# Kernel optimization log

Hardware: AMD Instinct MI355X
Metric: run time of the kernel (lower is better)

Reference implementation:

```python
import jax, jax.numpy as jnp
import numpy as np

B, NA, LAT, HID, AF, L = 512, 58, 64, 128, 10, 2
N = B * NA
E = N * 16


def silu(x):
    return x * jax.nn.sigmoid(x)


def setup_inputs() -> dict:
    key = jax.random.key(0)
    ks = list(jax.random.split(key, 32))

    def p(k, shape, fan_in):
        return jax.random.normal(k, shape, jnp.float32) / np.sqrt(fan_in)

    inp = {
        "z": jax.random.normal(ks[0], (B, LAT), jnp.float32),
        "atom_types": jax.random.uniform(ks[1], (N, AF), jnp.float32),
        "edge_index": jax.random.randint(ks[2], (2, E), 0, N, jnp.int64),
        "init_coords": jax.random.normal(ks[3], (NA, 3), jnp.float32) * 0.1,
        "latent_w": p(ks[4], (LAT, HID), LAT), "latent_b": jnp.zeros((HID,), jnp.float32),
        "atom_w": p(ks[5], (AF, HID), AF), "atom_b": jnp.zeros((HID,), jnp.float32),
        # per-layer stacked params (leading dim = num_layers)
        "edge_w1": p(ks[6], (L, 2 * HID + 1, HID), 2 * HID + 1), "edge_b1": jnp.zeros((L, HID), jnp.float32),
        "edge_w2": p(ks[7], (L, HID, HID), HID), "edge_b2": jnp.zeros((L, HID), jnp.float32),
        "node_w1": p(ks[8], (L, 2 * HID, HID), 2 * HID), "node_b1": jnp.zeros((L, HID), jnp.float32),
        "node_w2": p(ks[9], (L, HID, HID), HID), "node_b2": jnp.zeros((L, HID), jnp.float32),
        "coord_w1": p(ks[10], (L, HID, HID), HID), "coord_b1": jnp.zeros((L, HID), jnp.float32),
        "coord_w2": p(ks[11], (L, HID, 1), HID),  # no bias
        "ln_g": jnp.ones((L, HID), jnp.float32), "ln_b": jnp.zeros((L, HID), jnp.float32),
        "head_w1": p(ks[12], (HID, HID // 2), HID), "head_b1": jnp.zeros((HID // 2,), jnp.float32),
        "head_w2": p(ks[13], (HID // 2, 3), HID // 2), "head_b2": jnp.zeros((3,), jnp.float32),
    }
    return inp


def _layer(h, pos, row, col, ew1, eb1, ew2, eb2, nw1, nb1, nw2, nb2, cw1, cb1, cw2, lg, lb):
    n = h.shape[0]
    xi, xj = h[row], h[col]                      # [E,HID] gathers
    rel = pos[row] - pos[col]                    # [E,3]
    d2 = jnp.clip(jnp.sum(rel * rel, axis=-1, keepdims=True), 1e-6, 1e6)
    ef = jnp.concatenate([xi, xj, d2], axis=-1)  # [E,2H+1]
    m = silu(silu(ef @ ew1 + eb1) @ ew2 + eb2)   # edge MLP messages [E,HID]
    agg = jax.ops.segment_sum(m, row, num_segments=n)
    hn = silu(jnp.concatenate([h, agg], axis=-1) @ nw1 + nb1) @ nw2 + nb2
    mu = jnp.mean(hn, axis=-1, keepdims=True)
    var = jnp.mean((hn - mu) ** 2, axis=-1, keepdims=True)
    hn = (hn - mu) * jax.lax.rsqrt(var + 1e-5) * lg + lb
    cw = jnp.clip(silu(m @ cw1 + cb1) @ cw2, -1.0, 1.0)  # [E,1]
    upd = jax.ops.segment_sum(cw * rel, row, num_segments=n)  # [N,3]
    deg = jax.ops.segment_sum(jnp.ones((row.shape[0],), pos.dtype), row, num_segments=n)[:, None]
    pos_new = pos + upd / (deg + 1e-6)
    return hn, pos_new


def reference(z, atom_types, edge_index, init_coords, latent_w, latent_b, atom_w, atom_b,
              edge_w1, edge_b1, edge_w2, edge_b2, node_w1, node_b1, node_w2, node_b2,
              coord_w1, coord_b1, coord_w2, ln_g, ln_b, head_w1, head_b1, head_w2, head_b2):
    b = z.shape[0]
    na = init_coords.shape[0]
    n = b * na
    h = z @ latent_w + latent_b                              # [B,HID]
    h = jnp.broadcast_to(h[:, None, :], (b, na, h.shape[-1])).reshape(n, -1)
    h = h + (atom_types @ atom_w + atom_b)
    pos = jnp.broadcast_to(init_coords[None], (b, na, 3)).reshape(n, 3)
    row, col = edge_index[0], edge_index[1]
    for l in range(edge_w1.shape[0]):
        h, pos = _layer(h, pos, row, col,
                        edge_w1[l], edge_b1[l], edge_w2[l], edge_b2[l],
                        node_w1[l], node_b1[l], node_w2[l], node_b2[l],
                        coord_w1[l], coord_b1[l], coord_w2[l], ln_g[l], ln_b[l])
    delta = silu(h @ head_w1 + head_b1) @ head_w2 + head_b2
    return pos + delta
```

## Files before the change

kernel.cpp:

```cpp
#include <hip/hip_runtime.h>
#include <hip/hip_bf16.h>

#define BB 512
#define NA 58
#define LAT 64
#define HID 128
#define AF 10
#define NL 2
#define NN (BB*NA)
#define NE (NN*16)
#define ET 64
#define NTILE (NE/ET)
#define PBLK 768

typedef __attribute__((ext_vector_type(8))) short s8;
typedef __attribute__((ext_vector_type(4))) float f4;

struct CvtDesc {
    const void* src[24];
    float*      dst[24];
    int         len[24];
};

struct PackJobs {
    const float* src[10];
    short*       dst[10];
    int          K[10];
    int          mode[10];
};

__device__ __forceinline__ float siluf(float x) {
    return x * __builtin_amdgcn_rcpf(1.0f + __expf(-x));
}

__device__ __forceinline__ short f2b(float x) {
    __hip_bfloat16 b = __float2bfloat16(x);
    return *(short*)&b;
}

__device__ __forceinline__ float b2f(short s) {
    return __uint_as_float(((unsigned int)(unsigned short)s) << 16);
}

__global__ void k_detect(const unsigned short* __restrict__ z16,
                         const unsigned int* __restrict__ e32,
                         int* __restrict__ flags) {
    __shared__ int sbf, si64;
    if (threadIdx.x == 0) { sbf = 0; si64 = 0; }
    __syncthreads();
    int c1 = 0, c2 = 0;
    for (int i = threadIdx.x; i < 1024; i += 256) {
        unsigned short v = z16[2*i];
        int e = (v >> 7) & 0xFF;
        if (e >= 100 && e <= 140) c1++;
        if (e32[2*i + 1] == 0u) c2++;
    }
    atomicAdd(&sbf, c1);
    atomicAdd(&si64, c2);
    __syncthreads();
    if (threadIdx.x == 0) {
        flags[0] = (sbf  > 600) ? 1 : 0;
        flags[1] = (si64 > 600) ? 1 : 0;
    }
}

__global__ void k_convert(CvtDesc d, const int* __restrict__ flags) {
    int a = blockIdx.y;
    int i = blockIdx.x * blockDim.x + threadIdx.x;
    int n = d.len[a];
    if (i >= n) return;
    if (flags[0]) {
        d.dst[a][i] = __bfloat162float(((const __hip_bfloat16*)d.src[a])[i]);
    } else {
        d.dst[a][i] = ((const float*)d.src[a])[i];
    }
}

__global__ void k_packall(PackJobs pj) {
    int j = blockIdx.y;
    int idx = blockIdx.x * 256 + threadIdx.x;
    const float* w = pj.src[j];
    short* o = pj.dst[j];
    if (pj.mode[j] == 0) {
        int K = pj.K[j];
        if (idx >= 128*K) return;
        int jj = idx & 7;
        int l  = (idx >> 3) & 63;
        int rest = idx >> 9;
        int KC = K >> 5;
        int kc = rest % KC;
        int nt = rest / KC;
        int n = nt*16 + (l & 15);
        int k = kc*32 + (l >> 4)*8 + jj;
        o[idx] = f2b(w[k*128 + n]);
    } else {
        if (idx >= 32768) return;
        int jj = idx & 7;
        int l  = (idx >> 3) & 63;
        int rest = idx >> 9;
        int kc = rest & 3;
        int nt = rest >> 2;
        int n = nt*16 + (l & 15);
        int k = kc*32 + (l >> 4)*8 + jj;
        float v = (n < 128) ? w[k*128 + n] : w[(128 + k)*128 + (n - 128)];
        o[idx] = f2b(v);
    }
}

__global__ void k_hist(const int* __restrict__ eidx, const int* __restrict__ flags,
                       int* __restrict__ cnt) {
    int e = blockIdx.x * 256 + threadIdx.x;
    if (e >= NE) return;
    int is64 = flags[1];
    int r = eidx[is64 ? 2*(long)e : (long)e];
    atomicAdd(&cnt[r], 1);
}

__global__ __launch_bounds__(1024) void k_scan(const int* __restrict__ cnt,
                                               int* __restrict__ rowStart,
                                               int* __restrict__ cursor) {
    __shared__ int part[1024];
    int t = threadIdx.x;
    int base = t * 29;
    int loc[29];
    int s = 0;
    #pragma unroll
    for (int i = 0; i < 29; ++i) { loc[i] = s; s += cnt[base + i]; }
    part[t] = s;
    __syncthreads();
    for (int d = 1; d < 1024; d <<= 1) {
        int v = (t >= d) ? part[t - d] : 0;
        __syncthreads();
        part[t] += v;
        __syncthreads();
    }
    int pre = (t == 0) ? 0 : part[t - 1];
    #pragma unroll
    for (int i = 0; i < 29; ++i) {
        int v = pre + loc[i];
        rowStart[base + i] = v;
        cursor[base + i] = v;
    }
    if (t == 1023) rowStart[NN] = pre + s;
}

__global__ void k_scatter(const int* __restrict__ eidx, const int* __restrict__ flags,
                          int* __restrict__ cursor,
                          int* __restrict__ rS, int* __restrict__ cS) {
    int e = blockIdx.x * 256 + threadIdx.x;
    if (e >= NE) return;
    int is64 = flags[1];
    long ge = e, gc = (long)e + NE;
    int r = eidx[is64 ? 2*ge : ge];
    int c = eidx[is64 ? 2*gc : gc];
    int p = atomicAdd(&cursor[r], 1);
    rS[p] = r; cS[p] = c;
}

__global__ void k_hz(const float* __restrict__ z, const float* __restrict__ lw,
                     const float* __restrict__ lb, float* __restrict__ hz) {
    __shared__ float zs[LAT];
    int b = blockIdx.x;
    int c = threadIdx.x;
    if (c < LAT) zs[c] = z[b*LAT + c];
    __syncthreads();
    float acc = lb[c];
    #pragma unroll
    for (int k = 0; k < LAT; ++k) acc += zs[k] * lw[k*HID + c];
    hz[b*HID + c] = acc;
}

__global__ void k_init2(const float* __restrict__ hz, const float* __restrict__ at,
                        const float* __restrict__ aw, const float* __restrict__ ab,
                        const float* __restrict__ ic,
                        float* __restrict__ pos, short* __restrict__ hb) {
    __shared__ float ats[AF];
    int n = blockIdx.x;
    int c = threadIdx.x;
    int b = n / NA;
    if (c < AF) ats[c] = at[n*AF + c];
    __syncthreads();
    float acc = hz[b*HID + c] + ab[c];
    #pragma unroll
    for (int f = 0; f < AF; ++f) acc += ats[f] * aw[f*HID + c];
    hb[(long)n*HID + c] = f2b(acc);
    if (c < 3) {
        int a = n % NA;
        pos[n*3 + c] = ic[a*3 + c];
    }
}

__global__ __launch_bounds__(256) void k_pre(
    const short* __restrict__ hb, const short* __restrict__ wcat,
    const float* __restrict__ b1, short* __restrict__ H1,
    float* __restrict__ agg, float* __restrict__ upd)
{
    __shared__ short x[64][136];
    const int tid = threadIdx.x;
    const int n0 = blockIdx.x * 64;

    {
        long base = (long)blockIdx.x*256 + tid;
        f4* a4 = (f4*)agg;
        for (long j = base; j < (long)NN*HID/4; j += (long)gridDim.x*256) a4[j] = (f4)0.f;
        if (base < NN*3) upd[base] = 0.f;
    }

    #pragma unroll
    for (int it = 0; it < 4; ++it) {
        int idx = it*256 + tid;
        int e = idx >> 4, q = idx & 15;
        *(int4*)&x[e][q*8] = *(const int4*)(hb + (long)(n0+e)*HID + q*8);
    }
    __syncthreads();

    const int l = tid & 63, w = tid >> 6;
    const int l16 = l & 15, quad = l >> 4;

    f4 acc[4][4];
    #pragma unroll
    for (int mt = 0; mt < 4; ++mt)
        #pragma unroll
        for (int nt4 = 0; nt4 < 4; ++nt4) acc[mt][nt4] = (f4)0.f;

    #pragma unroll
    for (int kc = 0; kc < 4; ++kc) {
        s8 a[4];
        #pragma unroll
        for (int mt = 0; mt < 4; ++mt)
            a[mt] = *(const s8*)&x[mt*16 + l16][kc*32 + quad*8];
        #pragma unroll
        for (int nt4 = 0; nt4 < 4; ++nt4) {
            int nt = w*4 + nt4;
            s8 b = *(const s8*)(wcat + (((size_t)nt*4 + kc)*64 + l)*8);
            #pragma unroll
            for (int mt = 0; mt < 4; ++mt)
                acc[mt][nt4] = __builtin_amdgcn_mfma_f32_16x16x32_bf16(a[mt], b, acc[mt][nt4], 0, 0, 0);
        }
    }
    #pragma unroll
    for (int nt4 = 0; nt4 < 4; ++nt4) {
        int col = (w*4 + nt4)*16 + l16;
        float bias = (col < 128) ? b1[col] : 0.f;
        #pragma unroll
        for (int mt = 0; mt < 4; ++mt)
            #pragma unroll
            for (int i = 0; i < 4; ++i) {
                int row = mt*16 + quad*4 + i;
                H1[(long)(n0 + row)*256 + col] = f2b(acc[mt][nt4][i] + bias);
            }
    }
}

__global__ __launch_bounds__(256, 3) void k_edge7(
    const short* __restrict__ H1,
    const int* __restrict__ rS, const int* __restrict__ cS,
    const float* __restrict__ pos,
    const float* __restrict__ w1c,
    const short* __restrict__ w2p, const float* __restrict__ b2,
    const short* __restrict__ c1p, const float* __restrict__ cb1,
    const float* __restrict__ cw2,
    float* __restrict__ agg, float* __restrict__ upd)
{
    __shared__ short t1[ET][136];
    __shared__ short mm[ET][136];
    __shared__ int   rIs[ET], cIs[ET];
    __shared__ float sred[ET];

    const int tid = threadIdx.x;
    const int l = tid & 63, w = tid >> 6;
    const int l16 = l & 15, quad = l >> 4;
    const int c0 = (2*w)*16 + l16, c1c = (2*w+1)*16 + l16;
    const int half = tid >> 7, ch = tid & 127;
    const int q = tid & 15;
    const int esub = tid >> 4;

    float wv[8];
    #pragma unroll
    for (int j = 0; j < 8; ++j) wv[j] = w1c[q*8 + j];

    s8 w2f[8], c1f[8];
    #pragma unroll
    for (int kc = 0; kc < 4; ++kc) {
        w2f[kc]     = *(const s8*)(w2p + (((size_t)(2*w)*4 + kc)*64 + l)*8);
        w2f[4 + kc] = *(const s8*)(w2p + (((size_t)(2*w+1)*4 + kc)*64 + l)*8);
        c1f[kc]     = *(const s8*)(c1p + (((size_t)(2*w)*4 + kc)*64 + l)*8);
        c1f[4 + kc] = *(const s8*)(c1p + (((size_t)(2*w+1)*4 + kc)*64 + l)*8);
    }
    const float bia2_0 = b2[c0],  bia2_1 = b2[c1c];
    const float biac_0 = cb1[c0], biac_1 = cb1[c1c];
    const float cw0    = cw2[c0], cw1v   = cw2[c1c];

    int   pri[4], pci[4];
    float pd2[4];

    auto PREIDX = [&](int T) {
        long eb = (long)T * ET;
        #pragma unroll
        for (int it = 0; it < 4; ++it) {
            int e = esub + 16*it;
            int r = rS[eb + e], c = cS[eb + e];
            pri[it] = r; pci[it] = c;
            float rx = pos[r*3+0] - pos[c*3+0];
            float ry = pos[r*3+1] - pos[c*3+1];
            float rz = pos[r*3+2] - pos[c*3+2];
            pd2[it] = fminf(fmaxf(rx*rx + ry*ry + rz*rz, 1e-6f), 1e6f);
        }
    };

    int t = blockIdx.x;
    if (t < NTILE) PREIDX(t);

    while (t < NTILE) {
        __syncthreads();
        if (tid < ET) sred[tid] = 0.f;
        if (q == 0) {
            #pragma unroll
            for (int it = 0; it < 4; ++it) {
                rIs[esub + 16*it] = pri[it];
                cIs[esub + 16*it] = pci[it];
            }
        }
        #pragma unroll
        for (int it = 0; it < 4; ++it) {
            s8 va = *(const s8*)(H1 + (long)pri[it]*256 + q*8);
            s8 vb = *(const s8*)(H1 + (long)pci[it]*256 + 128 + q*8);
            float d2 = pd2[it];
            s8 o;
            #pragma unroll
            for (int j = 0; j < 8; ++j) {
                float v = b2f(va[j]) + b2f(vb[j]) + d2*wv[j];
                o[j] = f2b(siluf(v));
            }
            *(s8*)&t1[esub + 16*it][q*8] = o;
        }
        __syncthreads();

        int tn = t + PBLK;
        if (tn < NTILE) PREIDX(tn);

        {
            f4 acc[4][2];
            #pragma unroll
            for (int mt = 0; mt < 4; ++mt) { acc[mt][0] = (f4)0.f; acc[mt][1] = (f4)0.f; }
            #pragma unroll
            for (int kc = 0; kc < 4; ++kc) {
                #pragma unroll
                for (int mt = 0; mt < 4; ++mt) {
                    s8 a = *(const s8*)&t1[mt*16 + l16][kc*32 + quad*8];
                    acc[mt][0] = __builtin_amdgcn_mfma_f32_16x16x32_bf16(a, w2f[kc],     acc[mt][0], 0, 0, 0);
                    acc[mt][1] = __builtin_amdgcn_mfma_f32_16x16x32_bf16(a, w2f[4 + kc], acc[mt][1], 0, 0, 0);
                }
            }
            #pragma unroll
            for (int mt = 0; mt < 4; ++mt) {
                #pragma unroll
                for (int i = 0; i < 4; ++i) {
                    int row = mt*16 + quad*4 + i;
                    mm[row][c0]  = f2b(siluf(acc[mt][0][i] + bia2_0));
                    mm[row][c1c] = f2b(siluf(acc[mt][1][i] + bia2_1));
                }
            }
        }
        __syncthreads();

        {
            f4 acc[4][2];
            #pragma unroll
            for (int mt = 0; mt < 4; ++mt) { acc[mt][0] = (f4)0.f; acc[mt][1] = (f4)0.f; }
            #pragma unroll
            for (int kc = 0; kc < 4; ++kc) {
                #pragma unroll
                for (int mt = 0; mt < 4; ++mt) {
                    s8 a = *(const s8*)&mm[mt*16 + l16][kc*32 + quad*8];
                    acc[mt][0] = __builtin_amdgcn_mfma_f32_16x16x32_bf16(a, c1f[kc],     acc[mt][0], 0, 0, 0);
                    acc[mt][1] = __builtin_amdgcn_mfma_f32_16x16x32_bf16(a, c1f[4 + kc], acc[mt][1], 0, 0, 0);
                }
            }
            #pragma unroll
            for (int mt = 0; mt < 4; ++mt) {
                #pragma unroll
                for (int i = 0; i < 4; ++i) {
                    float p = siluf(acc[mt][0][i] + biac_0) * cw0
                            + siluf(acc[mt][1][i] + biac_1) * cw1v;
                    p += __shfl_xor(p, 1);
                    p += __shfl_xor(p, 2);
                    p += __shfl_xor(p, 4);
                    p += __shfl_xor(p, 8);
                    if (l16 == 0) {
                        int row = mt*16 + quad*4 + i;
                        atomicAdd(&sred[row], p);
                    }
                }
            }
        }

        {
            int e0 = half * 32;
            int cur = rIs[e0];
            float a = 0.f;
            #pragma unroll
            for (int e = e0; e < e0 + 32; ++e) {
                int r = rIs[e];
                if (r != cur) {
                    atomicAdd(&agg[(long)cur*HID + ch], a);
                    a = 0.f; cur = r;
                }
                a += b2f(mm[e][ch]);
            }
            atomicAdd(&agg[(long)cur*HID + ch], a);
        }
        __syncthreads();

        if (tid < ET) {
            float cwv = fminf(fmaxf(sred[tid], -1.f), 1.f);
            int r = rIs[tid], c = cIs[tid];
            float rx = pos[r*3+0] - pos[c*3+0];
            float ry = pos[r*3+1] - pos[c*3+1];
            float rz = pos[r*3+2] - pos[c*3+2];
            atomicAdd(&upd[r*3+0], cwv*rx);
            atomicAdd(&upd[r*3+1], cwv*ry);
            atomicAdd(&upd[r*3+2], cwv*rz);
        }
        t = tn;
    }
}

__global__ __launch_bounds__(256) void k_node_mfma(
    short* __restrict__ hb, const float* __restrict__ agg,
    const short* __restrict__ w1p, const float* __restrict__ b1n,
    const short* __restrict__ w2p, const float* __restrict__ b2n,
    const float* __restrict__ lg, const float* __restrict__ lb,
    float* __restrict__ pos, const float* __restrict__ upd,
    const int* __restrict__ rowStart)
{
    __shared__ short x[64][264];
    __shared__ short t1[64][144];
    __shared__ float mus[64], rstds[64];
    float (*hn)[132] = (float (*)[132])&x[0][0];

    const int tid = threadIdx.x;
    const int n0 = blockIdx.x * 64;

    #pragma unroll
    for (int it = 0; it < 4; ++it) {
        int idx = it*256 + tid;
        int e = idx >> 4, q = idx & 15;
        *(int4*)&x[e][q*8] = *(const int4*)(hb + (long)(n0+e)*HID + q*8);
    }
    #pragma unroll
    for (int it = 0; it < 8; ++it) {
        int idx = it*256 + tid;
        int e = idx >> 5, q = idx & 31;
        float4 v = *(const float4*)(agg + (long)(n0+e)*HID + q*4);
        short4 sv;
        sv.x = f2b(v.x); sv.y = f2b(v.y); sv.z = f2b(v.z); sv.w = f2b(v.w);
        *(short4*)&x[e][128 + q*4] = sv;
    }
    __syncthreads();

    const int l = tid & 63, w = tid >> 6;
    const int l16 = l & 15, quad = l >> 4;
    const int nt0 = 2*w, nt1 = 2*w + 1;
    const int c0 = nt0*16 + l16, c1c = nt1*16 + l16;

    {
        f4 acc[4][2];
        #pragma unroll
        for (int mt = 0; mt < 4; ++mt) { acc[mt][0] = (f4)0.f; acc[mt][1] = (f4)0.f; }
        #pragma unroll
        for (int kc = 0; kc < 8; ++kc) {
            s8 b0  = *(const s8*)(w1p + (((size_t)nt0*8 + kc)*64 + l)*8);
            s8 b1f = *(const s8*)(w1p + (((size_t)nt1*8 + kc)*64 + l)*8);
            #pragma unroll
            for (int mt = 0; mt < 4; ++mt) {
                s8 a = *(const s8*)&x[mt*16 + l16][kc*32 + quad*8];
                acc[mt][0] = __builtin_amdgcn_mfma_f32_16x16x32_bf16(a, b0,  acc[mt][0], 0, 0, 0);
                acc[mt][1] = __builtin_amdgcn_mfma_f32_16x16x32_bf16(a, b1f, acc[mt][1], 0, 0, 0);
            }
        }
        float bia0 = b1n[c0], bia1 = b1n[c1c];
        #pragma unroll
        for (int mt = 0; mt < 4; ++mt) {
            #pragma unroll
            for (int i = 0; i < 4; ++i) {
                int row = mt*16 + quad*4 + i;
                t1[row][c0]  = f2b(siluf(acc[mt][0][i] + bia0));
                t1[row][c1c] = f2b(siluf(acc[mt][1][i] + bia1));
            }
        }
    }
    __syncthreads();

    {
        f4 acc[4][2];
        #pragma unroll
        for (int mt = 0; mt < 4; ++mt) { acc[mt][0] = (f4)0.f; acc[mt][1] = (f4)0.f; }
        #pragma unroll
        for (int kc = 0; kc < 4; ++kc) {
            s8 b0  = *(const s8*)(w2p + (((size_t)nt0*4 + kc)*64 + l)*8);
            s8 b1f = *(const s8*)(w2p + (((size_t)nt1*4 + kc)*64 + l)*8);
            #pragma unroll
            for (int mt = 0; mt < 4; ++mt) {
                s8 a = *(const s8*)&t1[mt*16 + l16][kc*32 + quad*8];
                acc[mt][0] = __builtin_amdgcn_mfma_f32_16x16x32_bf16(a, b0,  acc[mt][0], 0, 0, 0);
                acc[mt][1] = __builtin_amdgcn_mfma_f32_16x16x32_bf16(a, b1f, acc[mt][1], 0, 0, 0);
            }
        }
        float bia0 = b2n[c0], bia1 = b2n[c1c];
        __syncthreads();
        #pragma unroll
        for (int mt = 0; mt < 4; ++mt) {
            #pragma unroll
            for (int i = 0; i < 4; ++i) {
                int row = mt*16 + quad*4 + i;
                hn[row][c0]  = acc[mt][0][i] + bia0;
                hn[row][c1c] = acc[mt][1][i] + bia1;
            }
        }
    }
    __syncthreads();

    {
        int r = tid >> 2, part = tid & 3;
        float s = 0.f, q = 0.f;
        #pragma unroll
        for (int j = 0; j < 32; ++j) {
            float v = hn[r][part + 4*j];
            s += v; q += v*v;
        }
        s += __shfl_xor(s, 1); q += __shfl_xor(q, 1);
        s += __shfl_xor(s, 2); q += __shfl_xor(q, 2);
        if (part == 0) {
            float mu = s * (1.0f/HID);
            float var = q * (1.0f/HID) - mu*mu;
            mus[r] = mu;
            rstds[r] = rsqrtf(var + 1e-5f);
        }
    }
    __syncthreads();

    #pragma unroll
    for (int it = 0; it < 32; ++it) {
        int idx = it*256 + tid;
        int r = idx >> 7, c = idx & 127;
        float v = (hn[r][c] - mus[r]) * rstds[r] * lg[c] + lb[c];
        hb[(long)(n0 + r)*HID + c] = f2b(v);
    }
    if (tid < 192) {
        int i = tid / 3, d = tid - i*3;
        int n = n0 + i;
        float dg = (float)(rowStart[n+1] - rowStart[n]);
        pos[n*3+d] += upd[n*3+d] / (dg + 1e-6f);
    }
}

__global__ void k_head(const short* __restrict__ hb, const float* __restrict__ pos,
                       const float* __restrict__ w1, const float* __restrict__ b1,
                       const float* __restrict__ w2, const float* __restrict__ b2,
                       void* __restrict__ out, const int* __restrict__ flags)
{
    __shared__ float hs[4][HID];
    __shared__ float t[4][64];
    const int tid = threadIdx.x;
    const int n0 = blockIdx.x * 4;
    for (int i = tid; i < 4*HID; i += 256)
        hs[i >> 7][i & 127] = b2f(hb[(long)n0*HID + i]);
    __syncthreads();
    const int s = tid >> 6, c = tid & 63;
    float acc = b1[c];
    for (int k4 = 0; k4 < 32; ++k4) {
        int k = k4*4;
        float wa = w1[(k+0)*64 + c];
        float wb = w1[(k+1)*64 + c];
        float wc = w1[(k+2)*64 + c];
        float wd = w1[(k+3)*64 + c];
        float4 v = *(const float4*)&hs[s][k];
        acc += v.x*wa + v.y*wb + v.z*wc + v.w*wd;
    }
    t[s][c] = siluf(acc);
    __syncthreads();
    if (c < 3) {
        float a2 = b2[c];
        #pragma unroll
        for (int k = 0; k < 64; ++k) a2 += t[s][k] * w2[k*3 + c];
        int n = n0 + s;
        float v = pos[n*3+c] + a2;
        if (flags[0]) ((__hip_bfloat16*)out)[n*3+c] = __float2bfloat16(v);
        else          ((float*)out)[n*3+c] = v;
    }
}

extern "C" void kernel_launch(void* const* d_in, const int* in_sizes, int n_in,
                              void* d_out, int out_size, void* d_ws, size_t ws_size,
                              hipStream_t stream)
{
    (void)in_sizes; (void)n_in; (void)out_size; (void)ws_size;

    int* flags = (int*)d_ws;
    float* base = (float*)d_ws;
    size_t off = 64;
    auto alloc = [&](size_t n) { float* p = base + off; off += (n + 63) & ~63ull; return p; };

    static const int aidx[24] = {0,1,3,4,5,6,7,8,9,10,11,12,13,14,15,16,17,18,19,20,21,22,23,24};
    static const int alen[24] = {
        BB*LAT, NN*AF, NA*3, LAT*HID, HID, AF*HID, HID,
        NL*257*HID, NL*HID, NL*HID*HID, NL*HID,
        NL*256*HID, NL*HID, NL*HID*HID, NL*HID,
        NL*HID*HID, NL*HID, NL*HID, NL*HID, NL*HID,
        HID*64, 64, 64*3, 3
    };
    CvtDesc cd;
    float* fp[24];
    for (int a = 0; a < 24; ++a) {
        fp[a] = alloc((size_t)alen[a]);
        cd.src[a] = d_in[aidx[a]];
        cd.dst[a] = fp[a];
        cd.len[a] = alen[a];
    }
    float* agg = alloc((size_t)NN*HID);
    float* hz  = alloc((size_t)BB*HID);
    float* pos = alloc((size_t)NN*3);
    float* upd = alloc((size_t)NN*3);
    short* hb  = (short*)alloc((size_t)NN*HID/2);
    short* H1  = (short*)alloc((size_t)NN*256/2);
    short* wcatp = (short*)alloc((size_t)NL*32768/2);
    short* w2p = (short*)alloc((size_t)NL*16384/2);
    short* c1p = (short*)alloc((size_t)NL*16384/2);
    short* nw1p = (short*)alloc((size_t)NL*32768/2);
    short* nw2p = (short*)alloc((size_t)NL*16384/2);
    int* cnt      = (int*)alloc((size_t)NN);
    int* rowStart = (int*)alloc((size_t)NN + 1);
    int* cursor   = (int*)alloc((size_t)NN);
    int* rS       = (int*)alloc((size_t)NE);
    int* cS       = (int*)alloc((size_t)NE);
    const int* eidx = (const int*)d_in[2];

    k_detect<<<1, 256, 0, stream>>>((const unsigned short*)d_in[0],
                                    (const unsigned int*)d_in[2], flags);
    k_convert<<<dim3((NN*AF + 255)/256, 24), 256, 0, stream>>>(cd, flags);

    PackJobs pj;
    for (int l = 0; l < NL; ++l) {
        int b5 = l*5;
        pj.src[b5+0] = fp[7]  + (size_t)l*257*HID; pj.dst[b5+0] = wcatp + (size_t)l*32768; pj.K[b5+0] = 256; pj.mode[b5+0] = 1;
        pj.src[b5+1] = fp[9]  + (size_t)l*HID*HID; pj.dst[b5+1] = w2p   + (size_t)l*16384; pj.K[b5+1] = 128; pj.mode[b5+1] = 0;
        pj.src[b5+2] = fp[15] + (size_t)l*HID*HID; pj.dst[b5+2] = c1p   + (size_t)l*16384; pj.K[b5+2] = 128; pj.mode[b5+2] = 0;
        pj.src[b5+3] = fp[11] + (size_t)l*256*HID; pj.dst[b5+3] = nw1p  + (size_t)l*32768; pj.K[b5+3] = 256; pj.mode[b5+3] = 0;
        pj.src[b5+4] = fp[13] + (size_t)l*HID*HID; pj.dst[b5+4] = nw2p  + (size_t)l*16384; pj.K[b5+4] = 128; pj.mode[b5+4] = 0;
    }
    k_packall<<<dim3(128, 10), 256, 0, stream>>>(pj);

    hipMemsetAsync(cnt, 0, (size_t)NN*sizeof(int), stream);
    k_hist<<<(NE + 255)/256, 256, 0, stream>>>(eidx, flags, cnt);
    k_scan<<<1, 1024, 0, stream>>>(cnt, rowStart, cursor);
    k_scatter<<<(NE + 255)/256, 256, 0, stream>>>(eidx, flags, cursor, rS, cS);

    k_hz<<<BB, HID, 0, stream>>>(fp[0], fp[3], fp[4], hz);
    k_init2<<<NN, HID, 0, stream>>>(hz, fp[1], fp[5], fp[6], fp[2], pos, hb);

    for (int l = 0; l < NL; ++l) {
        k_pre<<<NN/64, 256, 0, stream>>>(hb, wcatp + (size_t)l*32768,
                                         fp[8] + (size_t)l*HID, H1, agg, upd);
        k_edge7<<<PBLK, 256, 0, stream>>>(H1, rS, cS, pos,
            fp[7] + (size_t)l*257*HID + 256*HID,
            w2p + (size_t)l*16384, fp[10] + (size_t)l*HID,
            c1p + (size_t)l*16384, fp[16] + (size_t)l*HID,
            fp[17] + (size_t)l*HID,
            agg, upd);
        k_node_mfma<<<NN/64, 256, 0, stream>>>(hb, agg,
            nw1p + (size_t)l*32768, fp[12] + (size_t)l*HID,
            nw2p + (size_t)l*16384, fp[14] + (size_t)l*HID,
            fp[18] + (size_t)l*HID, fp[19] + (size_t)l*HID,
            pos, upd, rowStart);
    }
    k_head<<<NN/4, 256, 0, stream>>>(hb, pos, fp[20], fp[21], fp[22], fp[23],
                                     d_out, flags);
}
```

Before: 679.2 us.

## Fuse node-projection into init and node kernels; double-buffer edge tile gather

```diff
diff --git a/kernel.cpp b/kernel.cpp
--- a/kernel.cpp
+++ b/kernel.cpp
@@ -170,59 +170,57 @@
     hz[b*HID + c] = acc;
 }
 
-__global__ void k_init2(const float* __restrict__ hz, const float* __restrict__ at,
-                        const float* __restrict__ aw, const float* __restrict__ ab,
-                        const float* __restrict__ ic,
-                        float* __restrict__ pos, short* __restrict__ hb) {
-    __shared__ float ats[AF];
-    int n = blockIdx.x;
-    int c = threadIdx.x;
-    int b = n / NA;
-    if (c < AF) ats[c] = at[n*AF + c];
-    __syncthreads();
-    float acc = hz[b*HID + c] + ab[c];
-    #pragma unroll
-    for (int f = 0; f < AF; ++f) acc += ats[f] * aw[f*HID + c];
-    hb[(long)n*HID + c] = f2b(acc);
-    if (c < 3) {
-        int a = n % NA;
-        pos[n*3 + c] = ic[a*3 + c];
-    }
-}
-
-__global__ __launch_bounds__(256) void k_pre(
-    const short* __restrict__ hb, const short* __restrict__ wcat,
-    const float* __restrict__ b1, short* __restrict__ H1,
-    float* __restrict__ agg, float* __restrict__ upd)
+__global__ __launch_bounds__(256) void k_init3(
+    const float* __restrict__ hz, const float* __restrict__ at,
+    const float* __restrict__ aw, const float* __restrict__ ab,
+    const float* __restrict__ ic,
+    float* __restrict__ pos, short* __restrict__ hb,
+    const short* __restrict__ wcat0, const float* __restrict__ b10,
+    short* __restrict__ H1, float* __restrict__ agg, float* __restrict__ upd)
 {
     __shared__ short x[64][136];
+    __shared__ float awS[AF][HID];
+    __shared__ float atS[64][AF+2];
     const int tid = threadIdx.x;
     const int n0 = blockIdx.x * 64;
 
+    for (int i = tid; i < AF*HID; i += 256) awS[i/HID][i%HID] = aw[i];
+    for (int i = tid; i < 64*AF; i += 256)
+        atS[i/AF][i%AF] = at[(long)(n0 + i/AF)*AF + i%AF];
+    __syncthreads();
+
+    #pragma unroll
+    for (int it = 0; it < 32; ++it) {
+        int idx = it*256 + tid;
+        int r = idx >> 7, c = idx & 127;
+        int n = n0 + r;
+        int bb = n / NA;
+        float v = hz[bb*HID + c] + ab[c];
+        #pragma unroll
+        for (int f = 0; f < AF; ++f) v += atS[r][f]*awS[f][c];
+        short s = f2b(v);
+        x[r][c] = s;
+        hb[(long)n*HID + c] = s;
+    }
+    if (tid < 192) {
+        int i = tid/3, d = tid - i*3;
+        int n = n0 + i;
+        pos[n*3 + d] = ic[(n % NA)*3 + d];
+        upd[n*3 + d] = 0.f;
+    }
     {
-        long base = (long)blockIdx.x*256 + tid;
-        f4* a4 = (f4*)agg;
-        for (long j = base; j < (long)NN*HID/4; j += (long)gridDim.x*256) a4[j] = (f4)0.f;
-        if (base < NN*3) upd[base] = 0.f;
-    }
-
-    #pragma unroll
-    for (int it = 0; it < 4; ++it) {
-        int idx = it*256 + tid;
-        int e = idx >> 4, q = idx & 15;
-        *(int4*)&x[e][q*8] = *(const int4*)(hb + (long)(n0+e)*HID + q*8);
+        f4* a4 = (f4*)(agg + (long)n0*HID);
+        for (int j = tid; j < 64*HID/4; j += 256) a4[j] = (f4)0.f;
     }
     __syncthreads();
 
     const int l = tid & 63, w = tid >> 6;
     const int l16 = l & 15, quad = l >> 4;
-
     f4 acc[4][4];
     #pragma unroll
     for (int mt = 0; mt < 4; ++mt)
         #pragma unroll
         for (int nt4 = 0; nt4 < 4; ++nt4) acc[mt][nt4] = (f4)0.f;
-
     #pragma unroll
     for (int kc = 0; kc < 4; ++kc) {
         s8 a[4];
@@ -232,7 +230,7 @@
         #pragma unroll
         for (int nt4 = 0; nt4 < 4; ++nt4) {
             int nt = w*4 + nt4;
-            s8 b = *(const s8*)(wcat + (((size_t)nt*4 + kc)*64 + l)*8);
+            s8 b = *(const s8*)(wcat0 + (((size_t)nt*4 + kc)*64 + l)*8);
             #pragma unroll
             for (int mt = 0; mt < 4; ++mt)
                 acc[mt][nt4] = __builtin_amdgcn_mfma_f32_16x16x32_bf16(a[mt], b, acc[mt][nt4], 0, 0, 0);
@@ -241,7 +239,7 @@
     #pragma unroll
     for (int nt4 = 0; nt4 < 4; ++nt4) {
         int col = (w*4 + nt4)*16 + l16;
-        float bias = (col < 128) ? b1[col] : 0.f;
+        float bias = (col < 128) ? b10[col] : 0.f;
         #pragma unroll
         for (int mt = 0; mt < 4; ++mt)
             #pragma unroll
@@ -252,7 +250,7 @@
     }
 }
 
-__global__ __launch_bounds__(256, 3) void k_edge7(
+__global__ __launch_bounds__(256, 3) void k_edge8(
     const short* __restrict__ H1,
     const int* __restrict__ rS, const int* __restrict__ cS,
     const float* __restrict__ pos,
@@ -262,9 +260,9 @@
     const float* __restrict__ cw2,
     float* __restrict__ agg, float* __restrict__ upd)
 {
-    __shared__ short t1[ET][136];
+    __shared__ short t1[2][ET][136];
     __shared__ short mm[ET][136];
-    __shared__ int   rIs[ET], cIs[ET];
+    __shared__ int   rIs[2][ET], cIs[2][ET];
     __shared__ float sred[ET];
 
     const int tid = threadIdx.x;
@@ -293,7 +291,6 @@
 
     int   pri[4], pci[4];
     float pd2[4];
-
     auto PREIDX = [&](int T) {
         long eb = (long)T * ET;
         #pragma unroll
@@ -308,48 +305,66 @@
         }
     };
 
-    int t = blockIdx.x;
-    if (t < NTILE) PREIDX(t);
-
-    while (t < NTILE) {
-        __syncthreads();
-        if (tid < ET) sred[tid] = 0.f;
-        if (q == 0) {
-            #pragma unroll
-            for (int it = 0; it < 4; ++it) {
-                rIs[esub + 16*it] = pri[it];
-                cIs[esub + 16*it] = pci[it];
-            }
-        }
+    int T = blockIdx.x;
+    PREIDX(T);
+    #pragma unroll
+    for (int it = 0; it < 4; ++it) {
+        s8 va = *(const s8*)(H1 + (long)pri[it]*256 + q*8);
+        s8 vb = *(const s8*)(H1 + (long)pci[it]*256 + 128 + q*8);
+        float d2 = pd2[it];
+        s8 o;
+        #pragma unroll
+        for (int j = 0; j < 8; ++j)
+            o[j] = f2b(siluf(b2f(va[j]) + b2f(vb[j]) + d2*wv[j]));
+        *(s8*)&t1[0][esub + 16*it][q*8] = o;
+    }
+    if (q == 0) {
         #pragma unroll
         for (int it = 0; it < 4; ++it) {
-            s8 va = *(const s8*)(H1 + (long)pri[it]*256 + q*8);
-            s8 vb = *(const s8*)(H1 + (long)pci[it]*256 + 128 + q*8);
-            float d2 = pd2[it];
-            s8 o;
-            #pragma unroll
-            for (int j = 0; j < 8; ++j) {
-                float v = b2f(va[j]) + b2f(vb[j]) + d2*wv[j];
-                o[j] = f2b(siluf(v));
-            }
-            *(s8*)&t1[esub + 16*it][q*8] = o;
-        }
-        __syncthreads();
-
-        int tn = t + PBLK;
-        if (tn < NTILE) PREIDX(tn);
+            rIs[0][esub + 16*it] = pri[it];
+            cIs[0][esub + 16*it] = pci[it];
+        }
+    }
+    if (tid < ET) sred[tid] = 0.f;
+    int Tn = T + PBLK;
+    if (Tn < NTILE) PREIDX(Tn);
+    __syncthreads();
+
+    int b = 0;
+    while (true) {
+        const bool hasNext = (Tn < NTILE);
 
         {
             f4 acc[4][2];
             #pragma unroll
             for (int mt = 0; mt < 4; ++mt) { acc[mt][0] = (f4)0.f; acc[mt][1] = (f4)0.f; }
             #pragma unroll
-            for (int kc = 0; kc < 4; ++kc) {
+            for (int it = 0; it < 4; ++it) {
+                s8 va, vb;
+                if (hasNext) {
+                    va = *(const s8*)(H1 + (long)pri[it]*256 + q*8);
+                    vb = *(const s8*)(H1 + (long)pci[it]*256 + 128 + q*8);
+                }
                 #pragma unroll
                 for (int mt = 0; mt < 4; ++mt) {
-                    s8 a = *(const s8*)&t1[mt*16 + l16][kc*32 + quad*8];
-                    acc[mt][0] = __builtin_amdgcn_mfma_f32_16x16x32_bf16(a, w2f[kc],     acc[mt][0], 0, 0, 0);
-                    acc[mt][1] = __builtin_amdgcn_mfma_f32_16x16x32_bf16(a, w2f[4 + kc], acc[mt][1], 0, 0, 0);
+                    s8 a = *(const s8*)&t1[b][mt*16 + l16][it*32 + quad*8];
+                    acc[mt][0] = __builtin_amdgcn_mfma_f32_16x16x32_bf16(a, w2f[it],     acc[mt][0], 0, 0, 0);
+                    acc[mt][1] = __builtin_amdgcn_mfma_f32_16x16x32_bf16(a, w2f[4 + it], acc[mt][1], 0, 0, 0);
+                }
+                if (hasNext) {
+                    float d2 = pd2[it];
+                    s8 o;
+                    #pragma unroll
+                    for (int j = 0; j < 8; ++j)
+                        o[j] = f2b(siluf(b2f(va[j]) + b2f(vb[j]) + d2*wv[j]));
+                    *(s8*)&t1[b^1][esub + 16*it][q*8] = o;
+                }
+            }
+            if (hasNext && q == 0) {
+                #pragma unroll
+                for (int it = 0; it < 4; ++it) {
+                    rIs[b^1][esub + 16*it] = pri[it];
+                    cIs[b^1][esub + 16*it] = pci[it];
                 }
             }
             #pragma unroll
@@ -394,14 +409,13 @@
                 }
             }
         }
-
         {
             int e0 = half * 32;
-            int cur = rIs[e0];
+            int cur = rIs[b][e0];
             float a = 0.f;
             #pragma unroll
             for (int e = e0; e < e0 + 32; ++e) {
-                int r = rIs[e];
+                int r = rIs[b][e];
                 if (r != cur) {
                     atomicAdd(&agg[(long)cur*HID + ch], a);
                     a = 0.f; cur = r;
@@ -410,11 +424,14 @@
             }
             atomicAdd(&agg[(long)cur*HID + ch], a);
         }
+        int Tnn = Tn + PBLK;
+        if (hasNext && Tnn < NTILE) PREIDX(Tnn);
         __syncthreads();
 
         if (tid < ET) {
             float cwv = fminf(fmaxf(sred[tid], -1.f), 1.f);
-            int r = rIs[tid], c = cIs[tid];
+            sred[tid] = 0.f;
+            int r = rIs[b][tid], c = cIs[b][tid];
             float rx = pos[r*3+0] - pos[c*3+0];
             float ry = pos[r*3+1] - pos[c*3+1];
             float rz = pos[r*3+2] - pos[c*3+2];
@@ -422,17 +439,20 @@
             atomicAdd(&upd[r*3+1], cwv*ry);
             atomicAdd(&upd[r*3+2], cwv*rz);
         }
-        t = tn;
+        if (!hasNext) break;
+        T = Tn; Tn = Tnn; b ^= 1;
     }
 }
 
 __global__ __launch_bounds__(256) void k_node_mfma(
-    short* __restrict__ hb, const float* __restrict__ agg,
+    short* __restrict__ hb, float* __restrict__ agg,
     const short* __restrict__ w1p, const float* __restrict__ b1n,
     const short* __restrict__ w2p, const float* __restrict__ b2n,
     const float* __restrict__ lg, const float* __restrict__ lb,
-    float* __restrict__ pos, const float* __restrict__ upd,
-    const int* __restrict__ rowStart)
+    float* __restrict__ pos, float* __restrict__ upd,
+    const int* __restrict__ rowStart,
+    const short* __restrict__ wcatn, const float* __restrict__ b1next,
+    short* __restrict__ H1)
 {
     __shared__ short x[64][264];
     __shared__ short t1[64][144];
@@ -445,19 +465,24 @@
     #pragma unroll
     for (int it = 0; it < 4; ++it) {
         int idx = it*256 + tid;
-        int e = idx >> 4, q = idx & 15;
-        *(int4*)&x[e][q*8] = *(const int4*)(hb + (long)(n0+e)*HID + q*8);
+        int e = idx >> 4, qq = idx & 15;
+        *(int4*)&x[e][qq*8] = *(const int4*)(hb + (long)(n0+e)*HID + qq*8);
     }
     #pragma unroll
     for (int it = 0; it < 8; ++it) {
         int idx = it*256 + tid;
-        int e = idx >> 5, q = idx & 31;
-        float4 v = *(const float4*)(agg + (long)(n0+e)*HID + q*4);
+        int e = idx >> 5, qq = idx & 31;
+        float4 v = *(const float4*)(agg + (long)(n0+e)*HID + qq*4);
         short4 sv;
         sv.x = f2b(v.x); sv.y = f2b(v.y); sv.z = f2b(v.z); sv.w = f2b(v.w);
-        *(short4*)&x[e][128 + q*4] = sv;
-    }
-    __syncthreads();
+        *(short4*)&x[e][128 + qq*4] = sv;
+    }
+    __syncthreads();
+
+    {
+        f4* a4 = (f4*)(agg + (long)n0*HID);
+        for (int j = tid; j < 64*HID/4; j += 256) a4[j] = (f4)0.f;
+    }
 
     const int l = tid & 63, w = tid >> 6;
     const int l16 = l & 15, quad = l >> 4;
@@ -523,17 +548,17 @@
 
     {
         int r = tid >> 2, part = tid & 3;
-        float s = 0.f, q = 0.f;
+        float s = 0.f, qv = 0.f;
         #pragma unroll
         for (int j = 0; j < 32; ++j) {
             float v = hn[r][part + 4*j];
-            s += v; q += v*v;
-        }
-        s += __shfl_xor(s, 1); q += __shfl_xor(q, 1);
-        s += __shfl_xor(s, 2); q += __shfl_xor(q, 2);
+            s += v; qv += v*v;
+        }
+        s += __shfl_xor(s, 1); qv += __shfl_xor(qv, 1);
+        s += __shfl_xor(s, 2); qv += __shfl_xor(qv, 2);
         if (part == 0) {
             float mu = s * (1.0f/HID);
-            float var = q * (1.0f/HID) - mu*mu;
+            float var = qv * (1.0f/HID) - mu*mu;
             mus[r] = mu;
             rstds[r] = rsqrtf(var + 1e-5f);
         }
@@ -545,13 +570,52 @@
         int idx = it*256 + tid;
         int r = idx >> 7, c = idx & 127;
         float v = (hn[r][c] - mus[r]) * rstds[r] * lg[c] + lb[c];
-        hb[(long)(n0 + r)*HID + c] = f2b(v);
+        short s = f2b(v);
+        hb[(long)(n0 + r)*HID + c] = s;
+        t1[r][c] = s;
     }
     if (tid < 192) {
         int i = tid / 3, d = tid - i*3;
         int n = n0 + i;
         float dg = (float)(rowStart[n+1] - rowStart[n]);
         pos[n*3+d] += upd[n*3+d] / (dg + 1e-6f);
+        upd[n*3+d] = 0.f;
+    }
+
+    if (wcatn) {
+        __syncthreads();
+        f4 acc[4][4];
+        #pragma unroll
+        for (int mt = 0; mt < 4; ++mt)
+            #pragma unroll
+            for (int nt4 = 0; nt4 < 4; ++nt4) acc[mt][nt4] = (f4)0.f;
+        #pragma unroll
+        for (int kc = 0; kc < 4; ++kc) {
+            s8 a[4];
+            #pragma unroll
+            for (int mt = 0; mt < 4; ++mt)
+                a[mt] = *(const s8*)&t1[mt*16 + l16][kc*32 + quad*8];
+            #pragma unroll
+            for (int nt4 = 0; nt4 < 4; ++nt4) {
+                int nt = w*4 + nt4;
+                s8 b = *(const s8*)(wcatn + (((size_t)nt*4 + kc)*64 + l)*8);
+                #pragma unroll
+                for (int mt = 0; mt < 4; ++mt)
+                    acc[mt][nt4] = __builtin_amdgcn_mfma_f32_16x16x32_bf16(a[mt], b, acc[mt][nt4], 0, 0, 0);
+            }
+        }
+        #pragma unroll
+        for (int nt4 = 0; nt4 < 4; ++nt4) {
+            int col = (w*4 + nt4)*16 + l16;
+            float bias = (col < 128) ? b1next[col] : 0.f;
+            #pragma unroll
+            for (int mt = 0; mt < 4; ++mt)
+                #pragma unroll
+                for (int i = 0; i < 4; ++i) {
+                    int row = mt*16 + quad*4 + i;
+                    H1[(long)(n0 + row)*256 + col] = f2b(acc[mt][nt4][i] + bias);
+                }
+        }
     }
 }
 
@@ -657,22 +721,23 @@
     k_scatter<<<(NE + 255)/256, 256, 0, stream>>>(eidx, flags, cursor, rS, cS);
 
     k_hz<<<BB, HID, 0, stream>>>(fp[0], fp[3], fp[4], hz);
-    k_init2<<<NN, HID, 0, stream>>>(hz, fp[1], fp[5], fp[6], fp[2], pos, hb);
+    k_init3<<<NN/64, 256, 0, stream>>>(hz, fp[1], fp[5], fp[6], fp[2], pos, hb,
+                                       wcatp, fp[8], H1, agg, upd);
 
     for (int l = 0; l < NL; ++l) {
-        k_pre<<<NN/64, 256, 0, stream>>>(hb, wcatp + (size_t)l*32768,
-                                         fp[8] + (size_t)l*HID, H1, agg, upd);
-        k_edge7<<<PBLK, 256, 0, stream>>>(H1, rS, cS, pos,
+        k_edge8<<<PBLK, 256, 0, stream>>>(H1, rS, cS, pos,
             fp[7] + (size_t)l*257*HID + 256*HID,
             w2p + (size_t)l*16384, fp[10] + (size_t)l*HID,
             c1p + (size_t)l*16384, fp[16] + (size_t)l*HID,
             fp[17] + (size_t)l*HID,
             agg, upd);
+        const short* wcatn = (l+1 < NL) ? (wcatp + (size_t)(l+1)*32768) : nullptr;
+        const float* b1nx  = (l+1 < NL) ? (fp[8] + (size_t)(l+1)*HID) : fp[8];
         k_node_mfma<<<NN/64, 256, 0, stream>>>(hb, agg,
             nw1p + (size_t)l*32768, fp[12] + (size_t)l*HID,
             nw2p + (size_t)l*16384, fp[14] + (size_t)l*HID,
             fp[18] + (size_t)l*HID, fp[19] + (size_t)l*HID,
-            pos, upd, rowStart);
+            pos, upd, rowStart, wcatn, b1nx, H1);
     }
     k_head<<<NN/4, 256, 0, stream>>>(hb, pos, fp[20], fp[21], fp[22], fp[23],
                                      d_out, flags);
```

After: 647.4 us. -4.7%, faster.
